# Optimization experiments

Measured on AMD Instinct MI355X. Metric: run time of the kernel, lower is better.

Reference implementation:

```python
import jax, jax.numpy as jnp
import numpy as np

DILATIONS = [1, 2, 4, 8, 16, 32, 64, 128]
DEC_LEN = 256  # decoder_seq_len


def conv1x1(x, w, b):
    # x: [B, C, T], w: [O, C], b: [O]
    return jnp.einsum('oc,bct->bot', w, x) + b[None, :, None]


def causal_conv(x, w, b, dil):
    # x: [B, C, T], w: [O, C, K]; left-pad by (K-1)*dil => causal, same T out
    pad = (w.shape[-1] - 1) * dil
    y = jax.lax.conv_general_dilated(
        x, w, window_strides=(1,), padding=[(pad, 0)], rhs_dilation=(dil,),
        dimension_numbers=('NCH', 'OIH', 'NCH'))
    return y + b[None, :, None]


def setup_inputs() -> dict:
    key = jax.random.key(0)
    ks = jax.random.split(key, 14)
    L, Cin, Cout, Cmid, K, P = 8, 32, 64, 64, 2, 128
    B, T = 32, 4096
    s = 0.05  # keep activations in a sane range
    return {
        'x': jax.random.normal(ks[0], (B, Cin, T), dtype=jnp.float32),
        'pre_w': jax.random.normal(ks[1], (L, Cout, Cin)) * s,
        'pre_b': jax.random.normal(ks[2], (L, Cout)) * s,
        'filt_w': jax.random.normal(ks[3], (L, Cmid, Cout, K)) * s,
        'filt_b': jax.random.normal(ks[4], (L, Cmid)) * s,
        'gate_w': jax.random.normal(ks[5], (L, Cmid, Cout, K)) * s,
        'gate_b': jax.random.normal(ks[6], (L, Cmid)) * s,
        'post_w': jax.random.normal(ks[7], (L, Cout, Cmid)) * s,
        'post_b': jax.random.normal(ks[8], (L, Cout)) * s,
        'd1_w': jax.random.normal(ks[9], (P, Cout)) * s,
        'd1_b': jax.random.normal(ks[10], (P,)) * s,
        'd2_w': jax.random.normal(ks[11], (1, P)) * s,
        'd2_b': jax.random.normal(ks[12], (1,)) * s,
        'teacher_forcing_ratio': 1,
    }


def reference(x, pre_w, pre_b, filt_w, filt_b, gate_w, gate_b,
              post_w, post_b, d1_w, d1_b, d2_w, d2_b, teacher_forcing_ratio):
    # teacher_forcing_ratio == 1 path (vectorized teacher-forced forward)
    acc = None
    for i, dil in enumerate(DILATIONS):  # fixed small set of branches
        h = jax.nn.relu(conv1x1(x, pre_w[i], pre_b[i]))          # DenseConv pre
        f = causal_conv(h, filt_w[i], filt_b[i], dil)             # filter
        g = causal_conv(h, gate_w[i], gate_b[i], dil)             # gate
        s = jnp.tanh(f) * jax.nn.relu(g)                          # gated activation
        p = jax.nn.relu(conv1x1(s, post_w[i], post_b[i]))         # DenseConv post (skip output)
        acc = p if acc is None else acc + p
    out = jax.nn.relu(conv1x1(acc, d1_w, d1_b))                   # conv_dense1 (dropout=eval no-op)
    out = jax.nn.relu(conv1x1(out, d2_w, d2_b))                   # conv_dense2 -> [B, 1, T]
    out = jnp.transpose(out, (0, 2, 1))                           # [B, T, 1]
    return out[:, -DEC_LEN:, :]
```

## Files before the change

kernel.cpp:

```cpp
#include <hip/hip_runtime.h>

typedef _Float16 half2_t __attribute__((ext_vector_type(2)));
typedef _Float16 f16x8 __attribute__((ext_vector_type(8)));
typedef float f32x4 __attribute__((ext_vector_type(4)));

#define DEC 256
#define TFULL 4096
#define WIN0 3584
#define WLAYER_U32 11264
#define WTOT_U32 (8 * WLAYER_U32)
#define X16_U32 (32 * 512 * 16)
#define P_U32 (8 * 256 * 1024)
#define WS_NEED2 ((size_t)(WTOT_U32 + X16_U32 + P_U32) * 4)

#define HSTR 34
#define SSTR 36
#define HU (64 * HSTR)
#define LDS_U32 (HU + 32 * SSTR)

__device__ __forceinline__ float fast_tanh(float x) {
    float xa = fminf(fmaxf(x, -10.f), 10.f);
    float e = __expf(2.f * xa);
    return (e - 1.f) * __builtin_amdgcn_rcpf(e + 1.f);
}
__device__ __forceinline__ unsigned pk_rte(float a, float b) {
    union { _Float16 h[2]; unsigned u; } v;
    v.h[0] = (_Float16)a; v.h[1] = (_Float16)b; return v.u;
}
__device__ __forceinline__ half2_t h2(unsigned u) {
    return __builtin_bit_cast(half2_t, u);
}
__device__ __forceinline__ unsigned pkrtz(float a, float b) {
    return __builtin_bit_cast(unsigned, __builtin_amdgcn_cvt_pkrtz(a, b));
}

__global__ __launch_bounds__(512) void wavenet_prep16(
    const float* __restrict__ x,
    const float* __restrict__ pre_w,
    const float* __restrict__ fw, const float* __restrict__ gw,
    const float* __restrict__ pw, unsigned* __restrict__ ws)
{
    int idx = blockIdx.x * 512 + threadIdx.x;
    if (idx >= WTOT_U32 + X16_U32) return;
    unsigned v;
    if (idx < WTOT_U32) {
        int i = idx / WLAYER_U32;
        int r = idx - i * WLAYER_U32;
        if (r < 1024) {
            int kg = r >> 8, o = (r >> 2) & 63, e = r & 3;
            const float* p = pre_w + (i * 64 + o) * 32 + 8 * kg + 2 * e;
            v = pk_rte(p[0], p[1]);
        } else if (r < 5120) {
            int e2 = r - 1024;
            int kb = e2 >> 8, o = (e2 >> 2) & 63, e = e2 & 3;
            const float* p = fw + ((i * 64 + o) * 64 + 4 * kb + e) * 2;
            v = pk_rte(p[0], p[1]);
        } else if (r < 9216) {
            int e2 = r - 5120;
            int kb = e2 >> 8, o = (e2 >> 2) & 63, e = e2 & 3;
            const float* p = gw + ((i * 64 + o) * 64 + 4 * kb + e) * 2;
            v = pk_rte(p[0], p[1]);
        } else {
            int e3 = r - 9216;
            int kg = e3 >> 8, o = (e3 >> 2) & 63, e = e3 & 3;
            const float* p = pw + (i * 64 + o) * 64 + 8 * kg + 2 * e;
            v = pk_rte(p[0], p[1]);
        }
    } else {
        int e = idx - WTOT_U32;
        int b = e >> 13, r2 = e & 8191;
        int tw = r2 >> 4, cp = r2 & 15;
        const float* p = x + (size_t)(b * 32 + 2 * cp) * TFULL + WIN0 + tw;
        v = pk_rte(p[0], p[TFULL]);
    }
    ws[idx] = v;
}

__global__ __launch_bounds__(512) void wavenet_mfma2(
    const unsigned* __restrict__ wsu,
    const float* __restrict__ pre_b,
    const float* __restrict__ filt_b, const float* __restrict__ gate_b,
    const float* __restrict__ post_b,
    unsigned* __restrict__ pout)
{
    __shared__ __align__(16) unsigned lds[LDS_U32];

    const int tid = threadIdx.x;
    const int i = blockIdx.x >> 8;
    const int bt = blockIdx.x & 255;
    const int b = bt >> 3;
    const int tile = bt & 7;
    const int dil = 1 << i;
    const int off1 = (dil < 32) ? dil : 32;
    const int t0 = TFULL - DEC + tile * 32;

    const int lane = tid & 63;
    const int wv = __builtin_amdgcn_readfirstlane(tid >> 6);
    const int h4 = lane >> 4;
    const int ln = lane & 15;
    const int mt = wv >> 1;
    const int nt = wv & 1;

    const unsigned* xw = wsu + WTOT_U32 + b * 8192;
    const unsigned* wl = wsu + i * WLAYER_U32;

    {
        f16x8 a = *(const f16x8*)(wl + (h4 * 64 + mt * 16 + ln) * 4);
        float4 pb4 = *(const float4*)(pre_b + i * 64 + mt * 16 + 4 * h4);
#pragma unroll
        for (int ct2 = 0; ct2 < 2; ++ct2) {
            const int cw = (2 * (wv & 1) + ct2) * 16 + ln;
            int ta = (dil >= 32) ? ((cw < 32) ? (t0 - dil + cw) : (t0 + cw - 32))
                                 : (t0 - dil + cw);
            const int tw = (ta - WIN0) & 511;
            f16x8 bx = *(const f16x8*)(xw + tw * 16 + h4 * 4);
            f32x4 c = {0.f, 0.f, 0.f, 0.f};
            c = __builtin_amdgcn_mfma_f32_16x16x32_f16(a, bx, c, 0, 0, 0);
            uint2 hv;
            hv.x = pkrtz(fmaxf(c[0] + pb4.x, 0.f), fmaxf(c[1] + pb4.y, 0.f));
            hv.y = pkrtz(fmaxf(c[2] + pb4.z, 0.f), fmaxf(c[3] + pb4.w, 0.f));
            *(uint2*)&lds[cw * HSTR + mt * 8 + h4 * 2] = hv;
        }
    }
    __syncthreads();

    const int t = nt * 16 + ln;

    {
        f32x4 cf = {0.f, 0.f, 0.f, 0.f};
        f32x4 cg = {0.f, 0.f, 0.f, 0.f};
        const unsigned* fA = wl + 1024;
        const unsigned* gA = wl + 5120;
#pragma unroll
        for (int ki = 0; ki < 4; ++ki) {
            const int kbg = 4 * ki + h4;
            const int c2 = 8 * ki + 2 * h4;
            uint2 lo = *(const uint2*)&lds[t * HSTR + c2];
            uint2 hi = *(const uint2*)&lds[(t + off1) * HSTR + c2];
            uint4 bf;
            bf.x = (lo.x & 0xffffu) | (hi.x << 16);
            bf.y = (lo.x >> 16) | (hi.x & 0xffff0000u);
            bf.z = (lo.y & 0xffffu) | (hi.y << 16);
            bf.w = (lo.y >> 16) | (hi.y & 0xffff0000u);
            f16x8 bfrag = __builtin_bit_cast(f16x8, bf);
            f16x8 af = *(const f16x8*)(fA + (kbg * 64 + mt * 16 + ln) * 4);
            f16x8 ag = *(const f16x8*)(gA + (kbg * 64 + mt * 16 + ln) * 4);
            cf = __builtin_amdgcn_mfma_f32_16x16x32_f16(af, bfrag, cf, 0, 0, 0);
            cg = __builtin_amdgcn_mfma_f32_16x16x32_f16(ag, bfrag, cg, 0, 0, 0);
        }
        float4 fb = *(const float4*)(filt_b + i * 64 + mt * 16 + 4 * h4);
        float4 gb = *(const float4*)(gate_b + i * 64 + mt * 16 + 4 * h4);
        float s0 = fast_tanh(cf[0] + fb.x) * fmaxf(cg[0] + gb.x, 0.f);
        float s1 = fast_tanh(cf[1] + fb.y) * fmaxf(cg[1] + gb.y, 0.f);
        float s2 = fast_tanh(cf[2] + fb.z) * fmaxf(cg[2] + gb.z, 0.f);
        float s3 = fast_tanh(cf[3] + fb.w) * fmaxf(cg[3] + gb.w, 0.f);
        uint2 sv;
        sv.x = pkrtz(s0, s1);
        sv.y = pkrtz(s2, s3);
        *(uint2*)&lds[HU + t * SSTR + mt * 8 + h4 * 2] = sv;
    }
    __syncthreads();

    {
        f32x4 cp = {0.f, 0.f, 0.f, 0.f};
        const unsigned* pA = wl + 9216;
#pragma unroll
        for (int ki = 0; ki < 2; ++ki) {
            const int kg = 4 * ki + h4;
            f16x8 bs = *(const f16x8*)&lds[HU + t * SSTR + 4 * kg];
            f16x8 ap = *(const f16x8*)(pA + (kg * 64 + mt * 16 + ln) * 4);
            cp = __builtin_amdgcn_mfma_f32_16x16x32_f16(ap, bs, cp, 0, 0, 0);
        }
        float4 pb = *(const float4*)(post_b + i * 64 + mt * 16 + 4 * h4);
        float p0 = fmaxf(cp[0] + pb.x, 0.f);
        float p1 = fmaxf(cp[1] + pb.y, 0.f);
        float p2 = fmaxf(cp[2] + pb.z, 0.f);
        float p3 = fmaxf(cp[3] + pb.w, 0.f);
        const int op = mt * 8 + 2 * h4;
        unsigned* po = pout + (size_t)(i * 256 + bt) * 1024;
        po[op * 32 + t] = pkrtz(p0, p1);
        po[(op + 1) * 32 + t] = pkrtz(p2, p3);
    }
}

__global__ __launch_bounds__(512) void wavenet_head16(
    const unsigned* __restrict__ pin,
    const float* __restrict__ d1_w, const float* __restrict__ d1_b,
    const float* __restrict__ d2_w, const float* __restrict__ d2_b,
    float* __restrict__ out)
{
    __shared__ __align__(16) float accf[64 * 33];
    __shared__ float red[512];
    const int tid = threadIdx.x;
    const int bt = blockIdx.x;
    const int q = tid >> 5, tt = tid & 31;

    float a[4] = {0.f, 0.f, 0.f, 0.f};
#pragma unroll
    for (int l = 0; l < 8; ++l) {
        const unsigned* p = pin + (size_t)(l * 256 + bt) * 1024;
        half2_t h0 = h2(p[(2 * q) * 32 + tt]);
        half2_t h1 = h2(p[(2 * q + 1) * 32 + tt]);
        a[0] += (float)h0[0]; a[1] += (float)h0[1];
        a[2] += (float)h1[0]; a[3] += (float)h1[1];
    }
#pragma unroll
    for (int oo = 0; oo < 4; ++oo) accf[(4 * q + oo) * 33 + tt] = a[oo];
    __syncthreads();

    {
        const int pg = tid >> 5;
        float partial = 0.f;
#pragma unroll
        for (int pp = 0; pp < 8; ++pp) {
            const int p = pg * 8 + pp;
            float z = d1_b[p];
            const float4* w4 = (const float4*)(d1_w + p * 64);
#pragma unroll 4
            for (int c4 = 0; c4 < 16; ++c4) {
                float4 w = w4[c4];
                z = fmaf(w.x, accf[(c4 * 4 + 0) * 33 + tt], z);
                z = fmaf(w.y, accf[(c4 * 4 + 1) * 33 + tt], z);
                z = fmaf(w.z, accf[(c4 * 4 + 2) * 33 + tt], z);
                z = fmaf(w.w, accf[(c4 * 4 + 3) * 33 + tt], z);
            }
            partial = fmaf(d2_w[p], fmaxf(z, 0.f), partial);
        }
        red[pg * 32 + tt] = partial;
    }
    __syncthreads();
    if (tid < 32) {
        float sum = d2_b[0];
#pragma unroll
        for (int g = 0; g < 16; ++g) sum += red[g * 32 + tid];
        out[bt * 32 + tid] = fmaxf(sum, 0.f);
    }
}

#define HROW 164
#define SROW 33
__global__ __launch_bounds__(512) void wavenet_main(
    const float* __restrict__ x,
    const float* __restrict__ pre_w, const float* __restrict__ pre_b,
    const float* __restrict__ filt_w, const float* __restrict__ filt_b,
    const float* __restrict__ gate_w, const float* __restrict__ gate_b,
    const float* __restrict__ post_w, const float* __restrict__ post_b,
    const float* __restrict__ d1_w, const float* __restrict__ d1_b,
    const float* __restrict__ d2_w, const float* __restrict__ d2_b,
    float* __restrict__ out)
{
    __shared__ __align__(16) float h_s[64 * HROW];
    __shared__ __align__(16) float wbuf[20480];
    __shared__ __align__(16) float s_s[64 * SROW];
    const int tid = threadIdx.x;
    const int b = blockIdx.x >> 3;
    const int tile = blockIdx.x & 7;
    const int t0 = TFULL - DEC + tile * 32;
    const int lane = tid & 63;
    const int wv = __builtin_amdgcn_readfirstlane(tid >> 6);
    const int q = tid >> 5;
    const int tt = tid & 31;
    float accp[4] = {0.f, 0.f, 0.f, 0.f};
    for (int i = 0; i < 8; ++i) {
        const int dil = 1 << i;
        const int NC = 32 + dil;
        for (int m = tid; m < 8192; m += 512) {
            int c = m >> 7, rem = m & 127, o = rem >> 1, k = m & 1;
            wbuf[m] = filt_w[((i * 64 + o) * 64 + c) * 2 + k];
            wbuf[8192 + m] = gate_w[((i * 64 + o) * 64 + c) * 2 + k];
        }
        for (int m = tid; m < 4096; m += 512) {
            int c = m >> 6, o = m & 63;
            wbuf[16384 + m] = post_w[(i * 64 + o) * 64 + c];
        }
        __syncthreads();
        {
            const float* preb = pre_b + i * 64 + wv * 8;
            const float* prew = pre_w + (i * 64 + wv * 8) * 32;
            for (int col = lane; col < NC; col += 64) {
                int ta = t0 - dil + col;
                const float* xp = x + (size_t)b * 32 * TFULL + ta;
                float hacc[8];
#pragma unroll
                for (int r = 0; r < 8; ++r) hacc[r] = preb[r];
                for (int ci = 0; ci < 32; ++ci) {
                    float xv = xp[ci * TFULL];
#pragma unroll
                    for (int r = 0; r < 8; ++r)
                        hacc[r] = fmaf(prew[r * 32 + ci], xv, hacc[r]);
                }
#pragma unroll
                for (int r = 0; r < 8; ++r)
                    h_s[(wv * 8 + r) * HROW + col] = fmaxf(hacc[r], 0.f);
            }
        }
        __syncthreads();
        {
            float fa[4], ga[4];
#pragma unroll
            for (int oo = 0; oo < 4; ++oo) {
                fa[oo] = filt_b[i * 64 + q * 4 + oo];
                ga[oo] = gate_b[i * 64 + q * 4 + oo];
            }
            const float4* fw4 = (const float4*)wbuf;
            const float4* gw4 = (const float4*)(wbuf + 8192);
            const float* hrow0 = h_s + tt;
            const float* hrow1 = h_s + tt + dil;
#pragma unroll 4
            for (int c = 0; c < 64; ++c) {
                float4 f0 = fw4[c * 32 + q * 2];
                float4 f1 = fw4[c * 32 + q * 2 + 1];
                float4 g0 = gw4[c * 32 + q * 2];
                float4 g1 = gw4[c * 32 + q * 2 + 1];
                float h0 = hrow0[c * HROW];
                float h1 = hrow1[c * HROW];
                fa[0] = fmaf(f0.x, h0, fmaf(f0.y, h1, fa[0]));
                fa[1] = fmaf(f0.z, h0, fmaf(f0.w, h1, fa[1]));
                fa[2] = fmaf(f1.x, h0, fmaf(f1.y, h1, fa[2]));
                fa[3] = fmaf(f1.z, h0, fmaf(f1.w, h1, fa[3]));
                ga[0] = fmaf(g0.x, h0, fmaf(g0.y, h1, ga[0]));
                ga[1] = fmaf(g0.z, h0, fmaf(g0.w, h1, ga[1]));
                ga[2] = fmaf(g1.x, h0, fmaf(g1.y, h1, ga[2]));
                ga[3] = fmaf(g1.z, h0, fmaf(g1.w, h1, ga[3]));
            }
#pragma unroll
            for (int oo = 0; oo < 4; ++oo)
                s_s[(q * 4 + oo) * SROW + tt] = fast_tanh(fa[oo]) * fmaxf(ga[oo], 0.f);
        }
        __syncthreads();
        {
            float pa[4];
#pragma unroll
            for (int oo = 0; oo < 4; ++oo) pa[oo] = post_b[i * 64 + q * 4 + oo];
            const float4* pw4 = (const float4*)(wbuf + 16384);
#pragma unroll 4
            for (int c = 0; c < 64; ++c) {
                float4 pv = pw4[c * 16 + q];
                float sv = s_s[c * SROW + tt];
                pa[0] = fmaf(pv.x, sv, pa[0]);
                pa[1] = fmaf(pv.y, sv, pa[1]);
                pa[2] = fmaf(pv.z, sv, pa[2]);
                pa[3] = fmaf(pv.w, sv, pa[3]);
            }
#pragma unroll
            for (int oo = 0; oo < 4; ++oo) accp[oo] += fmaxf(pa[oo], 0.f);
        }
        __syncthreads();
    }
#pragma unroll
    for (int oo = 0; oo < 4; ++oo) s_s[(q * 4 + oo) * SROW + tt] = accp[oo];
    __syncthreads();
    {
        const int pg = tid >> 5;
        float partial = 0.f;
#pragma unroll
        for (int pp = 0; pp < 8; ++pp) {
            const int p = pg * 8 + pp;
            float z = d1_b[p];
            const float4* w4 = (const float4*)(d1_w + p * 64);
#pragma unroll 4
            for (int c4 = 0; c4 < 16; ++c4) {
                float4 w = w4[c4];
                z = fmaf(w.x, s_s[(c4 * 4 + 0) * SROW + tt], z);
                z = fmaf(w.y, s_s[(c4 * 4 + 1) * SROW + tt], z);
                z = fmaf(w.z, s_s[(c4 * 4 + 2) * SROW + tt], z);
                z = fmaf(w.w, s_s[(c4 * 4 + 3) * SROW + tt], z);
            }
            partial = fmaf(d2_w[p], fmaxf(z, 0.f), partial);
        }
        h_s[pg * 32 + tt] = partial;
    }
    __syncthreads();
    if (tid < 32) {
        float sum = d2_b[0];
#pragma unroll
        for (int g = 0; g < 16; ++g) sum += h_s[g * 32 + tid];
        out[b * DEC + tile * 32 + tid] = fmaxf(sum, 0.f);
    }
}

extern "C" void kernel_launch(void* const* d_in, const int* in_sizes, int n_in,
                              void* d_out, int out_size, void* d_ws, size_t ws_size,
                              hipStream_t stream)
{
    const float* x      = (const float*)d_in[0];
    const float* pre_w  = (const float*)d_in[1];
    const float* pre_b  = (const float*)d_in[2];
    const float* filt_w = (const float*)d_in[3];
    const float* filt_b = (const float*)d_in[4];
    const float* gate_w = (const float*)d_in[5];
    const float* gate_b = (const float*)d_in[6];
    const float* post_w = (const float*)d_in[7];
    const float* post_b = (const float*)d_in[8];
    const float* d1_w   = (const float*)d_in[9];
    const float* d1_b   = (const float*)d_in[10];
    const float* d2_w   = (const float*)d_in[11];
    const float* d2_b   = (const float*)d_in[12];
    float* out = (float*)d_out;

    if (ws_size >= WS_NEED2) {
        unsigned* ws = (unsigned*)d_ws;
        unsigned* part = ws + WTOT_U32 + X16_U32;
        wavenet_prep16<<<688, 512, 0, stream>>>(x, pre_w, filt_w, gate_w, post_w, ws);
        wavenet_mfma2<<<2048, 512, 0, stream>>>(
            ws, pre_b, filt_b, gate_b, post_b, part);
        wavenet_head16<<<256, 512, 0, stream>>>(
            part, d1_w, d1_b, d2_w, d2_b, out);
    } else {
        wavenet_main<<<256, 512, 0, stream>>>(
            x, pre_w, pre_b, filt_w, filt_b, gate_w, gate_b, post_w, post_b,
            d1_w, d1_b, d2_w, d2_b, out);
    }
}
```

Before: 30.60 us.

## Fuse per-layer MFMA kernel and head into one layer-looping kernel

Replaces the per-layer grid (one block per layer and time tile) plus a separate head kernel with a single kernel whose blocks loop over all eight layers. Skip outputs are accumulated in registers and reused through LDS for the dense head. This removes the global partial-sum buffer, its write/read traffic and one kernel launch. In exchange the grid shrinks eightfold and each block serializes the layers, reducing parallelism and latency hiding.

```diff
diff --git a/kernel.cpp b/kernel.cpp
--- a/kernel.cpp
+++ b/kernel.cpp
@@ -10,8 +10,7 @@
 #define WLAYER_U32 11264
 #define WTOT_U32 (8 * WLAYER_U32)
 #define X16_U32 (32 * 512 * 16)
-#define P_U32 (8 * 256 * 1024)
-#define WS_NEED2 ((size_t)(WTOT_U32 + X16_U32 + P_U32) * 4)
+#define WS_NEED ((size_t)(WTOT_U32 + X16_U32) * 4)
 
 #define HSTR 34
 #define SSTR 36
@@ -76,22 +75,21 @@
     ws[idx] = v;
 }
 
-__global__ __launch_bounds__(512) void wavenet_mfma2(
+__global__ __launch_bounds__(512) void wavenet_fused(
     const unsigned* __restrict__ wsu,
     const float* __restrict__ pre_b,
     const float* __restrict__ filt_b, const float* __restrict__ gate_b,
     const float* __restrict__ post_b,
-    unsigned* __restrict__ pout)
+    const float* __restrict__ d1_w, const float* __restrict__ d1_b,
+    const float* __restrict__ d2_w, const float* __restrict__ d2_b,
+    float* __restrict__ out)
 {
     __shared__ __align__(16) unsigned lds[LDS_U32];
 
     const int tid = threadIdx.x;
-    const int i = blockIdx.x >> 8;
-    const int bt = blockIdx.x & 255;
+    const int bt = blockIdx.x;
     const int b = bt >> 3;
     const int tile = bt & 7;
-    const int dil = 1 << i;
-    const int off1 = (dil < 32) ? dil : 32;
     const int t0 = TFULL - DEC + tile * 32;
 
     const int lane = tid & 63;
@@ -100,116 +98,100 @@
     const int ln = lane & 15;
     const int mt = wv >> 1;
     const int nt = wv & 1;
+    const int t = nt * 16 + ln;
 
     const unsigned* xw = wsu + WTOT_U32 + b * 8192;
-    const unsigned* wl = wsu + i * WLAYER_U32;
+
+    float acc[4] = {0.f, 0.f, 0.f, 0.f};
+
+    for (int i = 0; i < 8; ++i) {
+        const int dil = 1 << i;
+        const int off1 = (dil < 32) ? dil : 32;
+        const unsigned* wl = wsu + i * WLAYER_U32;
+
+        {
+            f16x8 a = *(const f16x8*)(wl + (h4 * 64 + mt * 16 + ln) * 4);
+            float4 pb4 = *(const float4*)(pre_b + i * 64 + mt * 16 + 4 * h4);
+#pragma unroll
+            for (int ct2 = 0; ct2 < 2; ++ct2) {
+                const int cw = (2 * nt + ct2) * 16 + ln;
+                int ta = (dil >= 32) ? ((cw < 32) ? (t0 - dil + cw) : (t0 + cw - 32))
+                                     : (t0 - dil + cw);
+                const int tw = (ta - WIN0) & 511;
+                f16x8 bx = *(const f16x8*)(xw + tw * 16 + h4 * 4);
+                f32x4 c = {0.f, 0.f, 0.f, 0.f};
+                c = __builtin_amdgcn_mfma_f32_16x16x32_f16(a, bx, c, 0, 0, 0);
+                uint2 hv;
+                hv.x = pkrtz(fmaxf(c[0] + pb4.x, 0.f), fmaxf(c[1] + pb4.y, 0.f));
+                hv.y = pkrtz(fmaxf(c[2] + pb4.z, 0.f), fmaxf(c[3] + pb4.w, 0.f));
+                *(uint2*)&lds[cw * HSTR + mt * 8 + h4 * 2] = hv;
+            }
+        }
+        __syncthreads();
+
+        {
+            f32x4 cf = {0.f, 0.f, 0.f, 0.f};
+            f32x4 cg = {0.f, 0.f, 0.f, 0.f};
+            const unsigned* fA = wl + 1024;
+            const unsigned* gA = wl + 5120;
+#pragma unroll
+            for (int ki = 0; ki < 4; ++ki) {
+                const int kbg = 4 * ki + h4;
+                const int c2 = 8 * ki + 2 * h4;
+                uint2 lo = *(const uint2*)&lds[t * HSTR + c2];
+                uint2 hi = *(const uint2*)&lds[(t + off1) * HSTR + c2];
+                uint4 bf;
+                bf.x = (lo.x & 0xffffu) | (hi.x << 16);
+                bf.y = (lo.x >> 16) | (hi.x & 0xffff0000u);
+                bf.z = (lo.y & 0xffffu) | (hi.y << 16);
+                bf.w = (lo.y >> 16) | (hi.y & 0xffff0000u);
+                f16x8 bfrag = __builtin_bit_cast(f16x8, bf);
+                f16x8 af = *(const f16x8*)(fA + (kbg * 64 + mt * 16 + ln) * 4);
+                f16x8 ag = *(const f16x8*)(gA + (kbg * 64 + mt * 16 + ln) * 4);
+                cf = __builtin_amdgcn_mfma_f32_16x16x32_f16(af, bfrag, cf, 0, 0, 0);
+                cg = __builtin_amdgcn_mfma_f32_16x16x32_f16(ag, bfrag, cg, 0, 0, 0);
+            }
+            float4 fb = *(const float4*)(filt_b + i * 64 + mt * 16 + 4 * h4);
+            float4 gb = *(const float4*)(gate_b + i * 64 + mt * 16 + 4 * h4);
+            float s0 = fast_tanh(cf[0] + fb.x) * fmaxf(cg[0] + gb.x, 0.f);
+            float s1 = fast_tanh(cf[1] + fb.y) * fmaxf(cg[1] + gb.y, 0.f);
+            float s2 = fast_tanh(cf[2] + fb.z) * fmaxf(cg[2] + gb.z, 0.f);
+            float s3 = fast_tanh(cf[3] + fb.w) * fmaxf(cg[3] + gb.w, 0.f);
+            uint2 sv;
+            sv.x = pkrtz(s0, s1);
+            sv.y = pkrtz(s2, s3);
+            *(uint2*)&lds[HU + t * SSTR + mt * 8 + h4 * 2] = sv;
+        }
+        __syncthreads();
+
+        {
+            f32x4 cp = {0.f, 0.f, 0.f, 0.f};
+            const unsigned* pA = wl + 9216;
+#pragma unroll
+            for (int ki = 0; ki < 2; ++ki) {
+                const int kg = 4 * ki + h4;
+                f16x8 bs = *(const f16x8*)&lds[HU + t * SSTR + 4 * kg];
+                f16x8 ap = *(const f16x8*)(pA + (kg * 64 + mt * 16 + ln) * 4);
+                cp = __builtin_amdgcn_mfma_f32_16x16x32_f16(ap, bs, cp, 0, 0, 0);
+            }
+            float4 pb = *(const float4*)(post_b + i * 64 + mt * 16 + 4 * h4);
+            acc[0] += fmaxf(cp[0] + pb.x, 0.f);
+            acc[1] += fmaxf(cp[1] + pb.y, 0.f);
+            acc[2] += fmaxf(cp[2] + pb.z, 0.f);
+            acc[3] += fmaxf(cp[3] + pb.w, 0.f);
+        }
+    }
+
+    __syncthreads();
+    float* accf = (float*)lds;
+    float* red = accf + 64 * 33;
+#pragma unroll
+    for (int k = 0; k < 4; ++k)
+        accf[(mt * 16 + 4 * h4 + k) * 33 + t] = acc[k];
+    __syncthreads();
 
     {
-        f16x8 a = *(const f16x8*)(wl + (h4 * 64 + mt * 16 + ln) * 4);
-        float4 pb4 = *(const float4*)(pre_b + i * 64 + mt * 16 + 4 * h4);
-#pragma unroll
-        for (int ct2 = 0; ct2 < 2; ++ct2) {
-            const int cw = (2 * (wv & 1) + ct2) * 16 + ln;
-            int ta = (dil >= 32) ? ((cw < 32) ? (t0 - dil + cw) : (t0 + cw - 32))
-                                 : (t0 - dil + cw);
-            const int tw = (ta - WIN0) & 511;
-            f16x8 bx = *(const f16x8*)(xw + tw * 16 + h4 * 4);
-            f32x4 c = {0.f, 0.f, 0.f, 0.f};
-            c = __builtin_amdgcn_mfma_f32_16x16x32_f16(a, bx, c, 0, 0, 0);
-            uint2 hv;
-            hv.x = pkrtz(fmaxf(c[0] + pb4.x, 0.f), fmaxf(c[1] + pb4.y, 0.f));
-            hv.y = pkrtz(fmaxf(c[2] + pb4.z, 0.f), fmaxf(c[3] + pb4.w, 0.f));
-            *(uint2*)&lds[cw * HSTR + mt * 8 + h4 * 2] = hv;
-        }
-    }
-    __syncthreads();
-
-    const int t = nt * 16 + ln;
-
-    {
-        f32x4 cf = {0.f, 0.f, 0.f, 0.f};
-        f32x4 cg = {0.f, 0.f, 0.f, 0.f};
-        const unsigned* fA = wl + 1024;
-        const unsigned* gA = wl + 5120;
-#pragma unroll
-        for (int ki = 0; ki < 4; ++ki) {
-            const int kbg = 4 * ki + h4;
-            const int c2 = 8 * ki + 2 * h4;
-            uint2 lo = *(const uint2*)&lds[t * HSTR + c2];
-            uint2 hi = *(const uint2*)&lds[(t + off1) * HSTR + c2];
-            uint4 bf;
-            bf.x = (lo.x & 0xffffu) | (hi.x << 16);
-            bf.y = (lo.x >> 16) | (hi.x & 0xffff0000u);
-            bf.z = (lo.y & 0xffffu) | (hi.y << 16);
-            bf.w = (lo.y >> 16) | (hi.y & 0xffff0000u);
-            f16x8 bfrag = __builtin_bit_cast(f16x8, bf);
-            f16x8 af = *(const f16x8*)(fA + (kbg * 64 + mt * 16 + ln) * 4);
-            f16x8 ag = *(const f16x8*)(gA + (kbg * 64 + mt * 16 + ln) * 4);
-            cf = __builtin_amdgcn_mfma_f32_16x16x32_f16(af, bfrag, cf, 0, 0, 0);
-            cg = __builtin_amdgcn_mfma_f32_16x16x32_f16(ag, bfrag, cg, 0, 0, 0);
-        }
-        float4 fb = *(const float4*)(filt_b + i * 64 + mt * 16 + 4 * h4);
-        float4 gb = *(const float4*)(gate_b + i * 64 + mt * 16 + 4 * h4);
-        float s0 = fast_tanh(cf[0] + fb.x) * fmaxf(cg[0] + gb.x, 0.f);
-        float s1 = fast_tanh(cf[1] + fb.y) * fmaxf(cg[1] + gb.y, 0.f);
-        float s2 = fast_tanh(cf[2] + fb.z) * fmaxf(cg[2] + gb.z, 0.f);
-        float s3 = fast_tanh(cf[3] + fb.w) * fmaxf(cg[3] + gb.w, 0.f);
-        uint2 sv;
-        sv.x = pkrtz(s0, s1);
-        sv.y = pkrtz(s2, s3);
-        *(uint2*)&lds[HU + t * SSTR + mt * 8 + h4 * 2] = sv;
-    }
-    __syncthreads();
-
-    {
-        f32x4 cp = {0.f, 0.f, 0.f, 0.f};
-        const unsigned* pA = wl + 9216;
-#pragma unroll
-        for (int ki = 0; ki < 2; ++ki) {
-            const int kg = 4 * ki + h4;
-            f16x8 bs = *(const f16x8*)&lds[HU + t * SSTR + 4 * kg];
-            f16x8 ap = *(const f16x8*)(pA + (kg * 64 + mt * 16 + ln) * 4);
-            cp = __builtin_amdgcn_mfma_f32_16x16x32_f16(ap, bs, cp, 0, 0, 0);
-        }
-        float4 pb = *(const float4*)(post_b + i * 64 + mt * 16 + 4 * h4);
-        float p0 = fmaxf(cp[0] + pb.x, 0.f);
-        float p1 = fmaxf(cp[1] + pb.y, 0.f);
-        float p2 = fmaxf(cp[2] + pb.z, 0.f);
-        float p3 = fmaxf(cp[3] + pb.w, 0.f);
-        const int op = mt * 8 + 2 * h4;
-        unsigned* po = pout + (size_t)(i * 256 + bt) * 1024;
-        po[op * 32 + t] = pkrtz(p0, p1);
-        po[(op + 1) * 32 + t] = pkrtz(p2, p3);
-    }
-}
-
-__global__ __launch_bounds__(512) void wavenet_head16(
-    const unsigned* __restrict__ pin,
-    const float* __restrict__ d1_w, const float* __restrict__ d1_b,
-    const float* __restrict__ d2_w, const float* __restrict__ d2_b,
-    float* __restrict__ out)
-{
-    __shared__ __align__(16) float accf[64 * 33];
-    __shared__ float red[512];
-    const int tid = threadIdx.x;
-    const int bt = blockIdx.x;
-    const int q = tid >> 5, tt = tid & 31;
-
-    float a[4] = {0.f, 0.f, 0.f, 0.f};
-#pragma unroll
-    for (int l = 0; l < 8; ++l) {
-        const unsigned* p = pin + (size_t)(l * 256 + bt) * 1024;
-        half2_t h0 = h2(p[(2 * q) * 32 + tt]);
-        half2_t h1 = h2(p[(2 * q + 1) * 32 + tt]);
-        a[0] += (float)h0[0]; a[1] += (float)h0[1];
-        a[2] += (float)h1[0]; a[3] += (float)h1[1];
-    }
-#pragma unroll
-    for (int oo = 0; oo < 4; ++oo) accf[(4 * q + oo) * 33 + tt] = a[oo];
-    __syncthreads();
-
-    {
-        const int pg = tid >> 5;
+        const int pg = tid >> 5, tt = tid & 31;
         float partial = 0.f;
 #pragma unroll
         for (int pp = 0; pp < 8; ++pp) {
@@ -398,14 +380,11 @@
     const float* d2_b   = (const float*)d_in[12];
     float* out = (float*)d_out;
 
-    if (ws_size >= WS_NEED2) {
+    if (ws_size >= WS_NEED) {
         unsigned* ws = (unsigned*)d_ws;
-        unsigned* part = ws + WTOT_U32 + X16_U32;
         wavenet_prep16<<<688, 512, 0, stream>>>(x, pre_w, filt_w, gate_w, post_w, ws);
-        wavenet_mfma2<<<2048, 512, 0, stream>>>(
-            ws, pre_b, filt_b, gate_b, post_b, part);
-        wavenet_head16<<<256, 512, 0, stream>>>(
-            part, d1_w, d1_b, d2_w, d2_b, out);
+        wavenet_fused<<<256, 512, 0, stream>>>(
+            ws, pre_b, filt_b, gate_b, post_b, d1_w, d1_b, d2_w, d2_b, out);
     } else {
         wavenet_main<<<256, 512, 0, stream>>>(
             x, pre_w, pre_b, filt_w, filt_b, gate_w, gate_b, post_w, post_b,
```

New measurement: 40.80 us. +33.3%, slower.

## Reorder filter/gate weight K layout to load B fragments directly, vectorize partial stores

Applied to the files above, without the earlier changes.

The prep kernel now packs the filter and gate weights tap-major, so each MFMA K-chunk holds channels from a single time row. The mfma kernel can then fetch its B fragment with one 16-byte LDS read instead of two 8-byte reads plus per-lane 16-bit shuffling. HSTR is raised to 36 for alignment. The skip-output partials are written as packed uint2 in a new interleaved layout, and the head kernel reads them with matching uint2 loads. The trade-off is more LDS per block and possible bank conflicts under the new stride.

```diff
diff --git a/kernel.cpp b/kernel.cpp
--- a/kernel.cpp
+++ b/kernel.cpp
@@ -11,9 +11,10 @@
 #define WTOT_U32 (8 * WLAYER_U32)
 #define X16_U32 (32 * 512 * 16)
 #define P_U32 (8 * 256 * 1024)
-#define WS_NEED2 ((size_t)(WTOT_U32 + X16_U32 + P_U32) * 4)
-
-#define HSTR 34
+#define XP_U32 (WTOT_U32 + X16_U32)
+#define WS_NEED2 ((size_t)(XP_U32 + P_U32) * 4)
+
+#define HSTR 36
 #define SSTR 36
 #define HU (64 * HSTR)
 #define LDS_U32 (HU + 32 * SSTR)
@@ -41,7 +42,7 @@
     const float* __restrict__ pw, unsigned* __restrict__ ws)
 {
     int idx = blockIdx.x * 512 + threadIdx.x;
-    if (idx >= WTOT_U32 + X16_U32) return;
+    if (idx >= XP_U32) return;
     unsigned v;
     if (idx < WTOT_U32) {
         int i = idx / WLAYER_U32;
@@ -50,16 +51,16 @@
             int kg = r >> 8, o = (r >> 2) & 63, e = r & 3;
             const float* p = pre_w + (i * 64 + o) * 32 + 8 * kg + 2 * e;
             v = pk_rte(p[0], p[1]);
-        } else if (r < 5120) {
-            int e2 = r - 1024;
+        } else if (r < 9216) {
+            const int isg = (r >= 5120);
+            int e2 = r - (isg ? 5120 : 1024);
             int kb = e2 >> 8, o = (e2 >> 2) & 63, e = e2 & 3;
-            const float* p = fw + ((i * 64 + o) * 64 + 4 * kb + e) * 2;
-            v = pk_rte(p[0], p[1]);
-        } else if (r < 9216) {
-            int e2 = r - 5120;
-            int kb = e2 >> 8, o = (e2 >> 2) & 63, e = e2 & 3;
-            const float* p = gw + ((i * 64 + o) * 64 + 4 * kb + e) * 2;
-            v = pk_rte(p[0], p[1]);
+            int m = kb >> 2, h4g = kb & 3;
+            int tap = m >> 1;
+            int c = 32 * (m & 1) + 8 * h4g + 2 * e;
+            const float* src = isg ? gw : fw;
+            const float* p = src + ((i * 64 + o) * 64 + c) * 2 + tap;
+            v = pk_rte(p[0], p[2]);
         } else {
             int e3 = r - 9216;
             int kg = e3 >> 8, o = (e3 >> 2) & 63, e = e3 & 3;
@@ -109,7 +110,7 @@
         float4 pb4 = *(const float4*)(pre_b + i * 64 + mt * 16 + 4 * h4);
 #pragma unroll
         for (int ct2 = 0; ct2 < 2; ++ct2) {
-            const int cw = (2 * (wv & 1) + ct2) * 16 + ln;
+            const int cw = (2 * nt + ct2) * 16 + ln;
             int ta = (dil >= 32) ? ((cw < 32) ? (t0 - dil + cw) : (t0 + cw - 32))
                                  : (t0 - dil + cw);
             const int tw = (ta - WIN0) & 511;
@@ -132,16 +133,10 @@
         const unsigned* fA = wl + 1024;
         const unsigned* gA = wl + 5120;
 #pragma unroll
-        for (int ki = 0; ki < 4; ++ki) {
-            const int kbg = 4 * ki + h4;
-            const int c2 = 8 * ki + 2 * h4;
-            uint2 lo = *(const uint2*)&lds[t * HSTR + c2];
-            uint2 hi = *(const uint2*)&lds[(t + off1) * HSTR + c2];
-            uint4 bf;
-            bf.x = (lo.x & 0xffffu) | (hi.x << 16);
-            bf.y = (lo.x >> 16) | (hi.x & 0xffff0000u);
-            bf.z = (lo.y & 0xffffu) | (hi.y << 16);
-            bf.w = (lo.y >> 16) | (hi.y & 0xffff0000u);
+        for (int m = 0; m < 4; ++m) {
+            const int kbg = 4 * m + h4;
+            const int row = (m >> 1) ? (t + off1) : t;
+            uint4 bf = *(const uint4*)&lds[row * HSTR + 16 * (m & 1) + 4 * h4];
             f16x8 bfrag = __builtin_bit_cast(f16x8, bf);
             f16x8 af = *(const f16x8*)(fA + (kbg * 64 + mt * 16 + ln) * 4);
             f16x8 ag = *(const f16x8*)(gA + (kbg * 64 + mt * 16 + ln) * 4);
@@ -172,14 +167,11 @@
             cp = __builtin_amdgcn_mfma_f32_16x16x32_f16(ap, bs, cp, 0, 0, 0);
         }
         float4 pb = *(const float4*)(post_b + i * 64 + mt * 16 + 4 * h4);
-        float p0 = fmaxf(cp[0] + pb.x, 0.f);
-        float p1 = fmaxf(cp[1] + pb.y, 0.f);
-        float p2 = fmaxf(cp[2] + pb.z, 0.f);
-        float p3 = fmaxf(cp[3] + pb.w, 0.f);
-        const int op = mt * 8 + 2 * h4;
+        uint2 o2;
+        o2.x = pkrtz(fmaxf(cp[0] + pb.x, 0.f), fmaxf(cp[1] + pb.y, 0.f));
+        o2.y = pkrtz(fmaxf(cp[2] + pb.z, 0.f), fmaxf(cp[3] + pb.w, 0.f));
         unsigned* po = pout + (size_t)(i * 256 + bt) * 1024;
-        po[op * 32 + t] = pkrtz(p0, p1);
-        po[(op + 1) * 32 + t] = pkrtz(p2, p3);
+        *(uint2*)&po[(mt * 4 + h4) * 64 + 2 * t] = o2;
     }
 }
 
@@ -199,10 +191,10 @@
 #pragma unroll
     for (int l = 0; l < 8; ++l) {
         const unsigned* p = pin + (size_t)(l * 256 + bt) * 1024;
-        half2_t h0 = h2(p[(2 * q) * 32 + tt]);
-        half2_t h1 = h2(p[(2 * q + 1) * 32 + tt]);
-        a[0] += (float)h0[0]; a[1] += (float)h0[1];
-        a[2] += (float)h1[0]; a[3] += (float)h1[1];
+        uint2 u = *(const uint2*)&p[q * 64 + 2 * tt];
+        half2_t u0 = h2(u.x), u1 = h2(u.y);
+        a[0] += (float)u0[0]; a[1] += (float)u0[1];
+        a[2] += (float)u1[0]; a[3] += (float)u1[1];
     }
 #pragma unroll
     for (int oo = 0; oo < 4; ++oo) accf[(4 * q + oo) * 33 + tt] = a[oo];
@@ -400,7 +392,7 @@
 
     if (ws_size >= WS_NEED2) {
         unsigned* ws = (unsigned*)d_ws;
-        unsigned* part = ws + WTOT_U32 + X16_U32;
+        unsigned* part = ws + XP_U32;
         wavenet_prep16<<<688, 512, 0, stream>>>(x, pre_w, filt_w, gate_w, post_w, ws);
         wavenet_mfma2<<<2048, 512, 0, stream>>>(
             ws, pre_b, filt_b, gate_b, post_b, part);
```

After: 30.65 us. Within noise of the previous version (+0.2%).
